# Optimization experiments

Measured on AMD Instinct MI355X. Metric: run time of the kernel, lower is better.

Reference implementation:

```python
import jax, jax.numpy as jnp
import numpy as np

# ---- fixed sizes ----
N_IN = 100_000          # total inner nodes
NODES_PER_INNER = 50    # nodes per inner graph
N_OUT = N_IN // NODES_PER_INNER          # 2000 outer nodes (= num inner graphs)
NODES_PER_OUTER = 125   # outer nodes per outer graph
B = N_OUT // NODES_PER_OUTER             # 16 graphs in the batch
DEG = 8
E_IN = N_IN * DEG        # 800_000 inner edges
E_OUT = N_OUT * DEG      # 16_000 outer edges
IN_FEATS = 64
OUT_FEATS = 64
H = 128                  # h_feats = [128]*6
NUM_CLASSES = 10


def _rand_edges(key, n_graphs, nodes_per_graph, edges_per_graph):
    """Random edges that stay inside each graph of a batched graph."""
    k1, k2 = jax.random.split(key)
    src_l = jax.random.randint(k1, (n_graphs, edges_per_graph), 0, nodes_per_graph)
    dst_l = jax.random.randint(k2, (n_graphs, edges_per_graph), 0, nodes_per_graph)
    off = (jnp.arange(n_graphs) * nodes_per_graph)[:, None]
    return ((src_l + off).reshape(-1).astype(jnp.int32),
            (dst_l + off).reshape(-1).astype(jnp.int32))


def setup_inputs() -> dict:
    key = jax.random.key(0)
    ks = jax.random.split(key, 24)
    inner_src, inner_dst = _rand_edges(ks[0], N_OUT, NODES_PER_INNER, E_IN // N_OUT)
    outer_src, outer_dst = _rand_edges(ks[1], B, NODES_PER_OUTER, E_OUT // B)

    def w(k, fan_in, fan_out):
        return jax.random.normal(k, (fan_in, fan_out), jnp.float32) * (1.0 / np.sqrt(fan_in))

    inp = {
        "in_layer_feat": jax.random.normal(ks[2], (N_IN, IN_FEATS), jnp.float32),
        "out_layer_feat": jax.random.normal(ks[3], (N_OUT, OUT_FEATS), jnp.float32),
        "inner_ew": jax.random.uniform(ks[4], (E_IN,), jnp.float32) + 0.5,
        "outer_ew": jax.random.uniform(ks[5], (E_OUT,), jnp.float32) + 0.5,
        "W1": w(ks[6], IN_FEATS, H),        "b1": jnp.zeros((H,), jnp.float32),
        "W2": w(ks[7], H, H),               "b2": jnp.zeros((H,), jnp.float32),
        "W3": w(ks[8], OUT_FEATS + H, H),   "b3": jnp.zeros((H,), jnp.float32),
        "W4": w(ks[9], H, H),               "b4": jnp.zeros((H,), jnp.float32),
        "W5": w(ks[10], H, H),              "b5": jnp.zeros((H,), jnp.float32),
        "W6": w(ks[11], H, H),              "b6": jnp.zeros((H,), jnp.float32),
        "Wc": w(ks[12], H, NUM_CLASSES),    "bc": jnp.zeros((NUM_CLASSES,), jnp.float32),
        "inner_src": inner_src, "inner_dst": inner_dst,
        "outer_src": outer_src, "outer_dst": outer_dst,
        "inner_node_graph": (jnp.arange(N_IN) // NODES_PER_INNER).astype(jnp.int32),
        "outer_node_graph": (jnp.arange(N_OUT) // NODES_PER_OUTER).astype(jnp.int32),
    }
    return inp


def graph_conv(src, dst, ew, x, W, b, n_nodes):
    """DGL GraphConv, norm='both', weighted aggregation, zero-in-degree allowed."""
    ones = jnp.ones(src.shape[0], x.dtype)
    deg_out = jnp.clip(jax.ops.segment_sum(ones, src, num_segments=n_nodes), 1.0)
    deg_in = jnp.clip(jax.ops.segment_sum(ones, dst, num_segments=n_nodes), 1.0)
    xs = x * jax.lax.rsqrt(deg_out)[:, None]                      # src normalization
    msg = xs[src] * ew[:, None]                                   # u_mul_e
    agg = jax.ops.segment_sum(msg, dst, num_segments=n_nodes)     # copy_e -> sum
    agg = agg * jax.lax.rsqrt(deg_in)[:, None]                    # dst normalization
    return agg @ W + b


def mean_nodes(h, node_graph, n_graphs, nodes_per_graph):
    return jax.ops.segment_sum(h, node_graph, num_segments=n_graphs) / nodes_per_graph


def reference(in_layer_feat, out_layer_feat, inner_ew, outer_ew,
              W1, b1, W2, b2, W3, b3, W4, b4, W5, b5, W6, b6, Wc, bc,
              inner_src, inner_dst, outer_src, outer_dst,
              inner_node_graph, outer_node_graph):
    # inner-graph message passing
    h = jax.nn.relu(graph_conv(inner_src, inner_dst, inner_ew, in_layer_feat, W1, b1, N_IN))
    h = jax.nn.relu(graph_conv(inner_src, inner_dst, inner_ew, h, W2, b2, N_IN))
    reduced = mean_nodes(h, inner_node_graph, N_OUT, float(NODES_PER_INNER))  # [N_OUT, H]
    merged = jnp.concatenate([out_layer_feat, reduced], axis=-1)              # [N_OUT, OUT_FEATS+H]
    # outer-graph message passing
    h = jax.nn.relu(graph_conv(outer_src, outer_dst, outer_ew, merged, W3, b3, N_OUT))
    h = jax.nn.relu(graph_conv(outer_src, outer_dst, outer_ew, h, W4, b4, N_OUT))
    h = jax.nn.relu(graph_conv(outer_src, outer_dst, outer_ew, h, W5, b5, N_OUT))
    h = jax.nn.relu(graph_conv(outer_src, outer_dst, outer_ew, h, W6, b6, N_OUT))
    hg = mean_nodes(h, outer_node_graph, B, float(NODES_PER_OUTER))           # [B, H]
    return hg @ Wc + bc                                                       # [B, NUM_CLASSES]
```

## Files before the change

### kernel.cpp

```cpp
#include <hip/hip_runtime.h>

#define NPI 50
#define EPI 400
#define NPO 125
#define EPO 1000
#define N_IN 100000
#define N_OUT 2000
#define NB 16
#define NC 10

typedef _Float16 half_t;
typedef _Float16 f16x8 __attribute__((ext_vector_type(8)));
typedef float f32x4 __attribute__((ext_vector_type(4)));

#define MFMA(a, b, c) __builtin_amdgcn_mfma_f32_16x16x32_f16(a, b, c, 0, 0, 0)

__device__ __forceinline__ void lds_barrier() {
    asm volatile("s_waitcnt lgkmcnt(0)" ::: "memory");
    __builtin_amdgcn_s_barrier();
}

__device__ __forceinline__ f16x8 lds_ld8(const half_t* base, int row, int k, int strideB) {
    return *(const f16x8*)((const char*)base + row * strideB + ((k * 2) ^ ((row & 7) << 4)));
}
__device__ __forceinline__ void lds_st1(half_t* base, int row, int col, int strideB, float v) {
    *(half_t*)((char*)base + row * strideB + ((col * 2) ^ ((row & 7) << 4))) = (half_t)v;
}
__device__ __forceinline__ void lds_st1h(half_t* base, int row, int col, int strideB, half_t v) {
    *(half_t*)((char*)base + row * strideB + ((col * 2) ^ ((row & 7) << 4))) = v;
}
__device__ __forceinline__ f16x8 scrS_ld8(const half_t* base, int row, int k, int strideB) {
    return *(const f16x8*)((const char*)base + row * strideB + ((k * 2) ^ ((row & 3) << 4)));
}
__device__ __forceinline__ void scrS_st1(half_t* base, int row, int col, int strideB, float v) {
    *(half_t*)((char*)base + row * strideB + ((col * 2) ^ ((row & 3) << 4))) = (half_t)v;
}

__global__ __launch_bounds__(256) void k_pre(
    const float* __restrict__ W1, const float* __restrict__ W2,
    const float* __restrict__ W3, const float* __restrict__ W4,
    const float* __restrict__ W5, const float* __restrict__ W6,
    half_t* __restrict__ WT1, half_t* __restrict__ WT2,
    half_t* __restrict__ WT3, half_t* __restrict__ WT4,
    half_t* __restrict__ WT5, half_t* __restrict__ WT6,
    const float* __restrict__ ew, const int* __restrict__ esrc,
    const int* __restrict__ edst, half_t* __restrict__ Aout)
{
    __shared__ float Af[NPO * NPO];
    __shared__ int cO[NPO], cI[NPO];
    __shared__ float rso[NPO], rsi[NPO];
    const int t = threadIdx.x;

    if (blockIdx.x < 384) {
        int i = blockIdx.x * 256 + t;
        const float* src; half_t* dst; int K;
        if      (i < 8192)  { src = W1; dst = WT1; K = 64; }
        else if (i < 24576) { src = W2; dst = WT2; K = 128; i -= 8192; }
        else if (i < 49152) { src = W3; dst = WT3; K = 192; i -= 24576; }
        else if (i < 65536) { src = W4; dst = WT4; K = 128; i -= 49152; }
        else if (i < 81920) { src = W5; dst = WT5; K = 128; i -= 65536; }
        else                { src = W6; dst = WT6; K = 128; i -= 81920; }
        int c = i & 127, k = i >> 7;
        dst[c * K + k] = (half_t)src[k * 128 + c];
        return;
    }

    const int g = blockIdx.x - 384;
    const int nb = g * NPO, eb = g * EPO;
    for (int i = t; i < NPO * NPO; i += 256) Af[i] = 0.f;
    if (t < NPO) { cO[t] = 0; cI[t] = 0; }
    __syncthreads();
    for (int e = t; e < EPO; e += 256) {
        int s = esrc[eb + e] - nb, d = edst[eb + e] - nb;
        atomicAdd(&Af[d * NPO + s], ew[eb + e]);
        atomicAdd(&cO[s], 1); atomicAdd(&cI[d], 1);
    }
    __syncthreads();
    if (t < NPO) {
        rso[t] = rsqrtf((float)max(cO[t], 1));
        rsi[t] = rsqrtf((float)max(cI[t], 1));
    }
    __syncthreads();
    for (int i = t; i < 128 * 16; i += 256) {
        int d = i >> 4, s0 = (i & 15) * 8;
        f16x8 v;
        #pragma unroll
        for (int j = 0; j < 8; j++) {
            int s = s0 + j;
            float x = (d < NPO && s < NPO) ? Af[d * NPO + s] * rsi[d] * rso[s] : 0.f;
            v[j] = (half_t)x;
        }
        *(f16x8*)&Aout[(size_t)g * 16384 + d * 128 + s0] = v;
    }
}

__global__ __launch_bounds__(256, 5) void k_inner(
    const float* __restrict__ X, const float* __restrict__ outfeat,
    const float* __restrict__ ew, const int* __restrict__ esrc,
    const int* __restrict__ edst,
    const half_t* __restrict__ WT1, const float* __restrict__ b1,
    const half_t* __restrict__ WT2, const float* __restrict__ b2,
    half_t* __restrict__ mergedT)
{
    __shared__ alignas(16) char smem[21504];
    half_t* R2  = (half_t*)smem;
    float*  Af  = (float*)smem;
    half_t* scr = (half_t*)(smem + 16384);
    float*  pool= (float*)(smem + 20480);
    int*    cO  = (int*)(smem + 20992);
    int*    cI  = (int*)(smem + 21248);

    const int g = blockIdx.x, t = threadIdx.x;
    const int w = t >> 6, l = t & 63, lr = l & 15, lk = l >> 4;
    const int nb = g * NPI, eb = g * EPI;
    half_t* scrw = scr + w * 512;

    float ofv = (t < 64) ? outfeat[(size_t)g * 64 + t] : 0.f;
    int s0e, d0e; float w0e;
    { int e = eb + t; s0e = esrc[e] - nb; d0e = edst[e] - nb; w0e = ew[e]; }
    int s1e = 0, d1e = 0; float w1e = 0.f;
    const bool e1v = (t + 256 < EPI);
    if (e1v) { int e = eb + t + 256; s1e = esrc[e] - nb; d1e = edst[e] - nb; w1e = ew[e]; }
    const int srow = t >> 2, qc = t & 3;
    f16x8 xh0 = {}, xh1 = {};
    if (srow < NPI) {
        const float* xp = &X[(size_t)(nb + srow) * 64 + qc * 16];
        float4 a = *(const float4*)(xp + 0), b = *(const float4*)(xp + 4);
        float4 c = *(const float4*)(xp + 8), d = *(const float4*)(xp + 12);
        xh0[0]=(half_t)a.x; xh0[1]=(half_t)a.y; xh0[2]=(half_t)a.z; xh0[3]=(half_t)a.w;
        xh0[4]=(half_t)b.x; xh0[5]=(half_t)b.y; xh0[6]=(half_t)b.z; xh0[7]=(half_t)b.w;
        xh1[0]=(half_t)c.x; xh1[1]=(half_t)c.y; xh1[2]=(half_t)c.z; xh1[3]=(half_t)c.w;
        xh1[4]=(half_t)d.x; xh1[5]=(half_t)d.y; xh1[6]=(half_t)d.z; xh1[7]=(half_t)d.w;
    }

    if (t < 64) { cO[t] = 0; cI[t] = 0; }
    if (t >= 64 && t < 192) pool[t - 64] = 0.f;
    for (int i = t; i < 4096; i += 256) Af[i] = 0.f;
    lds_barrier();

    atomicAdd(&Af[d0e * 64 + (s0e ^ ((d0e & 7) << 2))], w0e);
    atomicAdd(&cO[s0e], 1); atomicAdd(&cI[d0e], 1);
    if (e1v) {
        atomicAdd(&Af[d1e * 64 + (s1e ^ ((d1e & 7) << 2))], w1e);
        atomicAdd(&cO[s1e], 1); atomicAdd(&cI[d1e], 1);
    }
    lds_barrier();

    f16x8 afr[2];
    {
        const int r = w * 16 + lr;
        const int sw = (r & 7) << 2;
        const float rsi_l = rsqrtf((float)max(cI[r], 1));
        #pragma unroll
        for (int ks = 0; ks < 2; ks++) {
            const int c0 = ks * 32 + lk * 8;
            f32x4 v0 = *(const f32x4*)&Af[r * 64 + (c0 ^ sw)];
            f32x4 v1 = *(const f32x4*)&Af[r * 64 + ((c0 + 4) ^ sw)];
            f16x8 fr;
            #pragma unroll
            for (int j = 0; j < 4; j++)
                fr[j] = (half_t)(v0[j] * rsi_l * rsqrtf((float)max(cO[c0 + j], 1)));
            #pragma unroll
            for (int j = 0; j < 4; j++)
                fr[4 + j] = (half_t)(v1[j] * rsi_l * rsqrtf((float)max(cO[c0 + 4 + j], 1)));
            afr[ks] = fr;
        }
    }
    lds_barrier();

    #pragma unroll
    for (int i = 0; i < 8; i++) lds_st1h(R2, qc * 16 + i, srow, 128, xh0[i]);
    #pragma unroll
    for (int i = 0; i < 8; i++) lds_st1h(R2, qc * 16 + 8 + i, srow, 128, xh1[i]);
    lds_barrier();

    f32x4 hacc[8] = {};
    #pragma unroll
    for (int kf = 0; kf < 2; kf++) {
        f16x8 wb[8];
        #pragma unroll
        for (int nt = 0; nt < 8; nt++)
            wb[nt] = *(const f16x8*)&WT1[(nt * 16 + lr) * 64 + kf * 32 + lk * 8];
        #pragma unroll
        for (int j = 0; j < 2; j++) {
            const int ft = kf * 2 + j;
            f32x4 tacc = {};
            #pragma unroll
            for (int ks = 0; ks < 2; ks++) {
                f16x8 b = lds_ld8(R2, ft * 16 + lr, ks * 32 + lk * 8, 128);
                tacc = MFMA(afr[ks], b, tacc);
            }
            #pragma unroll
            for (int q = 0; q < 4; q++) scrS_st1(scrw, lk * 4 + q, j * 16 + lr, 64, tacc[q]);
        }
        f16x8 a1 = scrS_ld8(scrw, lr, lk * 8, 64);
        #pragma unroll
        for (int nt = 0; nt < 8; nt++) hacc[nt] = MFMA(a1, wb[nt], hacc[nt]);
    }
    lds_barrier();
    #pragma unroll
    for (int nt = 0; nt < 8; nt++) {
        int c = nt * 16 + lr;
        float bb = b1[c];
        #pragma unroll
        for (int q = 0; q < 4; q++)
            lds_st1(R2, c, w * 16 + lk * 4 + q, 128, fmaxf(hacc[nt][q] + bb, 0.f));
    }
    lds_barrier();

    f32x4 h2[8] = {};
    #pragma unroll
    for (int kf = 0; kf < 4; kf++) {
        f16x8 wb[8];
        #pragma unroll
        for (int nt = 0; nt < 8; nt++)
            wb[nt] = *(const f16x8*)&WT2[(nt * 16 + lr) * 128 + kf * 32 + lk * 8];
        #pragma unroll
        for (int j = 0; j < 2; j++) {
            const int ft = kf * 2 + j;
            f32x4 tacc = {};
            #pragma unroll
            for (int ks = 0; ks < 2; ks++) {
                f16x8 b = lds_ld8(R2, ft * 16 + lr, ks * 32 + lk * 8, 128);
                tacc = MFMA(afr[ks], b, tacc);
            }
            #pragma unroll
            for (int q = 0; q < 4; q++) scrS_st1(scrw, lk * 4 + q, j * 16 + lr, 64, tacc[q]);
        }
        f16x8 a1 = scrS_ld8(scrw, lr, lk * 8, 64);
        #pragma unroll
        for (int nt = 0; nt < 8; nt++) h2[nt] = MFMA(a1, wb[nt], h2[nt]);
    }
    #pragma unroll
    for (int nt = 0; nt < 8; nt++) {
        int c = nt * 16 + lr;
        float bb = b2[c];
        float ps = 0.f;
        #pragma unroll
        for (int q = 0; q < 4; q++) {
            int m = w * 16 + lk * 4 + q;
            float v = fmaxf(h2[nt][q] + bb, 0.f);
            ps += (m < NPI) ? v : 0.f;
        }
        ps += __shfl_xor(ps, 16);
        ps += __shfl_xor(ps, 32);
        if (lk == 0) atomicAdd(&pool[c], ps);
    }
    lds_barrier();
    {
        const int og = g / NPO, n = g - og * NPO;
        half_t* mT = mergedT + (size_t)og * 192 * 128 + n;
        if (t < 64) mT[(size_t)t * 128] = (half_t)ofv;
        else if (t < 192) mT[(size_t)t * 128] = (half_t)(pool[t - 64] * (1.f / NPI));
    }
}

template <int FIN>
__global__ __launch_bounds__(64) void k_layer(
    const half_t* __restrict__ Aout, const half_t* __restrict__ inT,
    const half_t* __restrict__ WT, const float* __restrict__ bias,
    half_t* __restrict__ outT)
{
    __shared__ alignas(16) half_t scrT[16 * FIN];
    __shared__ alignas(16) half_t hts[128 * 16];
    const int t = threadIdx.x, lr = t & 15, lk = t >> 4;
    const int og = blockIdx.x >> 3, r0 = (blockIdx.x & 7) * 16;
    const half_t* Ag = Aout + (size_t)og * 16384;
    const half_t* ig = inT + (size_t)og * FIN * 128;

    f16x8 af[4];
    #pragma unroll
    for (int ks = 0; ks < 4; ks++)
        af[ks] = *(const f16x8*)&Ag[(size_t)(r0 + lr) * 128 + ks * 32 + lk * 8];

    constexpr int NT = FIN / 16;
    #pragma unroll
    for (int nt = 0; nt < NT; nt++) {
        f32x4 tacc = {};
        #pragma unroll
        for (int ks = 0; ks < 4; ks++) {
            f16x8 b = *(const f16x8*)&ig[(size_t)(nt * 16 + lr) * 128 + ks * 32 + lk * 8];
            tacc = MFMA(af[ks], b, tacc);
        }
        #pragma unroll
        for (int q = 0; q < 4; q++)
            scrS_st1(scrT, lk * 4 + q, nt * 16 + lr, FIN * 2, tacc[q]);
    }

    f32x4 hacc[8] = {};
    #pragma unroll
    for (int ks2 = 0; ks2 < FIN / 32; ks2++) {
        f16x8 a1 = scrS_ld8(scrT, lr, ks2 * 32 + lk * 8, FIN * 2);
        #pragma unroll
        for (int nt2 = 0; nt2 < 8; nt2++) {
            f16x8 wb = *(const f16x8*)&WT[(size_t)(nt2 * 16 + lr) * FIN + ks2 * 32 + lk * 8];
            hacc[nt2] = MFMA(a1, wb, hacc[nt2]);
        }
    }
    #pragma unroll
    for (int nt2 = 0; nt2 < 8; nt2++) {
        int c = nt2 * 16 + lr;
        float bb = bias[c];
        #pragma unroll
        for (int q = 0; q < 4; q++)
            hts[c * 16 + lk * 4 + q] = (half_t)fmaxf(hacc[nt2][q] + bb, 0.f);
    }
    #pragma unroll
    for (int j = 0; j < 4; j++) {
        int id = t + j * 64;
        int f = id >> 1, i0 = (id & 1) * 8;
        f16x8 v = *(const f16x8*)&hts[f * 16 + i0];
        *(f16x8*)&outT[(size_t)og * 16384 + (size_t)f * 128 + r0 + i0] = v;
    }
}

__global__ __launch_bounds__(128) void k_pool(
    const half_t* __restrict__ h6T, const float* __restrict__ Wc,
    const float* __restrict__ bc, float* __restrict__ out)
{
    __shared__ float cls[NC];
    const int og = blockIdx.x, t = threadIdx.x;
    if (t < NC) cls[t] = 0.f;
    const half_t* hp = h6T + (size_t)og * 16384 + (size_t)t * 128;
    float s = 0.f;
    #pragma unroll
    for (int i = 0; i < 15; i++) {
        f16x8 v = *(const f16x8*)&hp[i * 8];
        #pragma unroll
        for (int j = 0; j < 8; j++) s += (float)v[j];
    }
    #pragma unroll
    for (int i = 120; i < 125; i++) s += (float)hp[i];
    const float val = s * (1.f / NPO);
    __syncthreads();
    {
        float p[NC];
        #pragma unroll
        for (int c = 0; c < NC; c++) p[c] = val * Wc[t * NC + c];
        #pragma unroll
        for (int off = 32; off >= 1; off >>= 1)
            #pragma unroll
            for (int c = 0; c < NC; c++) p[c] += __shfl_xor(p[c], off);
        if ((t & 63) == 0)
            #pragma unroll
            for (int c = 0; c < NC; c++) atomicAdd(&cls[c], p[c]);
    }
    __syncthreads();
    if (t < NC) out[og * NC + t] = cls[t] + bc[t];
}

extern "C" void kernel_launch(void* const* d_in, const int* in_sizes, int n_in,
                              void* d_out, int out_size, void* d_ws, size_t ws_size,
                              hipStream_t stream)
{
    const float* X       = (const float*)d_in[0];
    const float* outfeat = (const float*)d_in[1];
    const float* iew     = (const float*)d_in[2];
    const float* oew     = (const float*)d_in[3];
    const float* W1 = (const float*)d_in[4];  const float* b1 = (const float*)d_in[5];
    const float* W2 = (const float*)d_in[6];  const float* b2 = (const float*)d_in[7];
    const float* W3 = (const float*)d_in[8];  const float* b3 = (const float*)d_in[9];
    const float* W4 = (const float*)d_in[10]; const float* b4 = (const float*)d_in[11];
    const float* W5 = (const float*)d_in[12]; const float* b5 = (const float*)d_in[13];
    const float* W6 = (const float*)d_in[14]; const float* b6 = (const float*)d_in[15];
    const float* Wc = (const float*)d_in[16]; const float* bc = (const float*)d_in[17];
    const int* isrc = (const int*)d_in[18];   const int* idst = (const int*)d_in[19];
    const int* osrc = (const int*)d_in[20];   const int* odst = (const int*)d_in[21];

    char* base = (char*)d_ws;
    half_t* WT1 = (half_t*)(base + 0);
    half_t* WT2 = (half_t*)(base + 16384);
    half_t* WT3 = (half_t*)(base + 49152);
    half_t* WT4 = (half_t*)(base + 98304);
    half_t* WT5 = (half_t*)(base + 131072);
    half_t* WT6 = (half_t*)(base + 163840);
    half_t* AoutG   = (half_t*)(base + 196608);
    half_t* mergedT = (half_t*)(base + 720896);
    half_t* hTa     = (half_t*)(base + 1507328);
    half_t* hTb     = (half_t*)(base + 2031616);

    k_pre<<<400, 256, 0, stream>>>(W1, W2, W3, W4, W5, W6,
                                   WT1, WT2, WT3, WT4, WT5, WT6,
                                   oew, osrc, odst, AoutG);
    k_inner<<<N_OUT, 256, 0, stream>>>(X, outfeat, iew, isrc, idst,
                                       WT1, b1, WT2, b2, mergedT);
    k_layer<192><<<NB * 8, 64, 0, stream>>>(AoutG, mergedT, WT3, b3, hTa);
    k_layer<128><<<NB * 8, 64, 0, stream>>>(AoutG, hTa, WT4, b4, hTb);
    k_layer<128><<<NB * 8, 64, 0, stream>>>(AoutG, hTb, WT5, b5, hTa);
    k_layer<128><<<NB * 8, 64, 0, stream>>>(AoutG, hTa, WT6, b6, hTb);
    k_pool<<<NB, 128, 0, stream>>>(hTb, Wc, bc, (float*)d_out);
}
```

Before: 135.3 us.

## Fuse outer-graph layers and pooling into one persistent kernel with grid barriers

Replaces the four per-layer launches and the pooling launch with a single persistent 128-block kernel that uses global atomic-counter barriers between stages. The outer adjacency build and the W3-W6 transposes move into this kernel, and the adjacency is accumulated in global memory that a small pre-kernel zeroes. Each block now uses 4 waves, each computing a quarter of the output columns instead of one wave doing all of them. The aim is to remove several kernel launch gaps and tails on a short dependent chain, at the cost of spin-barrier overhead and global atomics for the adjacency.

```diff
diff --git a/kernel.cpp b/kernel.cpp
--- a/kernel.cpp
+++ b/kernel.cpp
@@ -8,6 +8,7 @@
 #define N_OUT 2000
 #define NB 16
 #define NC 10
+#define OB 128
 
 typedef _Float16 half_t;
 typedef _Float16 f16x8 __attribute__((ext_vector_type(8)));
@@ -36,62 +37,21 @@
     *(half_t*)((char*)base + row * strideB + ((col * 2) ^ ((row & 3) << 4))) = (half_t)v;
 }
 
-__global__ __launch_bounds__(256) void k_pre(
+__global__ __launch_bounds__(256) void k_preW12(
     const float* __restrict__ W1, const float* __restrict__ W2,
-    const float* __restrict__ W3, const float* __restrict__ W4,
-    const float* __restrict__ W5, const float* __restrict__ W6,
     half_t* __restrict__ WT1, half_t* __restrict__ WT2,
-    half_t* __restrict__ WT3, half_t* __restrict__ WT4,
-    half_t* __restrict__ WT5, half_t* __restrict__ WT6,
-    const float* __restrict__ ew, const int* __restrict__ esrc,
-    const int* __restrict__ edst, half_t* __restrict__ Aout)
+    int* __restrict__ zbase, int zcount)
 {
-    __shared__ float Af[NPO * NPO];
-    __shared__ int cO[NPO], cI[NPO];
-    __shared__ float rso[NPO], rsi[NPO];
-    const int t = threadIdx.x;
-
-    if (blockIdx.x < 384) {
-        int i = blockIdx.x * 256 + t;
-        const float* src; half_t* dst; int K;
-        if      (i < 8192)  { src = W1; dst = WT1; K = 64; }
-        else if (i < 24576) { src = W2; dst = WT2; K = 128; i -= 8192; }
-        else if (i < 49152) { src = W3; dst = WT3; K = 192; i -= 24576; }
-        else if (i < 65536) { src = W4; dst = WT4; K = 128; i -= 49152; }
-        else if (i < 81920) { src = W5; dst = WT5; K = 128; i -= 65536; }
-        else                { src = W6; dst = WT6; K = 128; i -= 81920; }
+    int i = blockIdx.x * 256 + threadIdx.x;
+    if (i < 8192) {
         int c = i & 127, k = i >> 7;
-        dst[c * K + k] = (half_t)src[k * 128 + c];
-        return;
-    }
-
-    const int g = blockIdx.x - 384;
-    const int nb = g * NPO, eb = g * EPO;
-    for (int i = t; i < NPO * NPO; i += 256) Af[i] = 0.f;
-    if (t < NPO) { cO[t] = 0; cI[t] = 0; }
-    __syncthreads();
-    for (int e = t; e < EPO; e += 256) {
-        int s = esrc[eb + e] - nb, d = edst[eb + e] - nb;
-        atomicAdd(&Af[d * NPO + s], ew[eb + e]);
-        atomicAdd(&cO[s], 1); atomicAdd(&cI[d], 1);
-    }
-    __syncthreads();
-    if (t < NPO) {
-        rso[t] = rsqrtf((float)max(cO[t], 1));
-        rsi[t] = rsqrtf((float)max(cI[t], 1));
-    }
-    __syncthreads();
-    for (int i = t; i < 128 * 16; i += 256) {
-        int d = i >> 4, s0 = (i & 15) * 8;
-        f16x8 v;
-        #pragma unroll
-        for (int j = 0; j < 8; j++) {
-            int s = s0 + j;
-            float x = (d < NPO && s < NPO) ? Af[d * NPO + s] * rsi[d] * rso[s] : 0.f;
-            v[j] = (half_t)x;
-        }
-        *(f16x8*)&Aout[(size_t)g * 16384 + d * 128 + s0] = v;
-    }
+        WT1[c * 64 + k] = (half_t)W1[k * 128 + c];
+    } else {
+        int ii = i - 8192;
+        int c = ii & 127, k = ii >> 7;
+        WT2[c * 128 + k] = (half_t)W2[k * 128 + c];
+    }
+    for (int j = i; j < zcount; j += 96 * 256) zbase[j] = 0;
 }
 
 __global__ __launch_bounds__(256, 5) void k_inner(
@@ -255,98 +215,177 @@
     }
 }
 
+__device__ __forceinline__ void gsync(int* ctr, int idx) {
+    __syncthreads();
+    if (threadIdx.x == 0) {
+        __threadfence();
+        atomicAdd(&ctr[idx], 1);
+        while (atomicAdd(&ctr[idx], 0) < OB) __builtin_amdgcn_s_sleep(2);
+        __threadfence();
+    }
+    __syncthreads();
+}
+
 template <int FIN>
-__global__ __launch_bounds__(64) void k_layer(
-    const half_t* __restrict__ Aout, const half_t* __restrict__ inT,
+__device__ __forceinline__ void do_layer(
+    const f16x8* af, const half_t* __restrict__ ig,
     const half_t* __restrict__ WT, const float* __restrict__ bias,
-    half_t* __restrict__ outT)
+    half_t* __restrict__ outg, int r0, half_t* scrT, half_t* hts,
+    int w, int lr, int lk, int t)
 {
-    __shared__ alignas(16) half_t scrT[16 * FIN];
-    __shared__ alignas(16) half_t hts[128 * 16];
-    const int t = threadIdx.x, lr = t & 15, lk = t >> 4;
-    const int og = blockIdx.x >> 3, r0 = (blockIdx.x & 7) * 16;
-    const half_t* Ag = Aout + (size_t)og * 16384;
-    const half_t* ig = inT + (size_t)og * FIN * 128;
-
-    f16x8 af[4];
-    #pragma unroll
-    for (int ks = 0; ks < 4; ks++)
-        af[ks] = *(const f16x8*)&Ag[(size_t)(r0 + lr) * 128 + ks * 32 + lk * 8];
-
-    constexpr int NT = FIN / 16;
-    #pragma unroll
-    for (int nt = 0; nt < NT; nt++) {
+    constexpr int TP = FIN / 64;
+    #pragma unroll
+    for (int tt = 0; tt < TP; tt++) {
+        const int ft = w * TP + tt;
         f32x4 tacc = {};
         #pragma unroll
         for (int ks = 0; ks < 4; ks++) {
-            f16x8 b = *(const f16x8*)&ig[(size_t)(nt * 16 + lr) * 128 + ks * 32 + lk * 8];
+            f16x8 b = *(const f16x8*)&ig[(size_t)(ft * 16 + lr) * 128 + ks * 32 + lk * 8];
             tacc = MFMA(af[ks], b, tacc);
         }
         #pragma unroll
         for (int q = 0; q < 4; q++)
-            scrS_st1(scrT, lk * 4 + q, nt * 16 + lr, FIN * 2, tacc[q]);
-    }
-
-    f32x4 hacc[8] = {};
+            scrS_st1(scrT, lk * 4 + q, ft * 16 + lr, FIN * 2, tacc[q]);
+    }
+    __syncthreads();
+    f32x4 hacc[2] = {};
     #pragma unroll
     for (int ks2 = 0; ks2 < FIN / 32; ks2++) {
         f16x8 a1 = scrS_ld8(scrT, lr, ks2 * 32 + lk * 8, FIN * 2);
         #pragma unroll
-        for (int nt2 = 0; nt2 < 8; nt2++) {
-            f16x8 wb = *(const f16x8*)&WT[(size_t)(nt2 * 16 + lr) * FIN + ks2 * 32 + lk * 8];
+        for (int nt2 = 0; nt2 < 2; nt2++) {
+            f16x8 wb = *(const f16x8*)&WT[(size_t)(w * 32 + nt2 * 16 + lr) * FIN
+                                          + ks2 * 32 + lk * 8];
             hacc[nt2] = MFMA(a1, wb, hacc[nt2]);
         }
     }
     #pragma unroll
-    for (int nt2 = 0; nt2 < 8; nt2++) {
-        int c = nt2 * 16 + lr;
+    for (int nt2 = 0; nt2 < 2; nt2++) {
+        int c = w * 32 + nt2 * 16 + lr;
         float bb = bias[c];
         #pragma unroll
         for (int q = 0; q < 4; q++)
             hts[c * 16 + lk * 4 + q] = (half_t)fmaxf(hacc[nt2][q] + bb, 0.f);
     }
-    #pragma unroll
-    for (int j = 0; j < 4; j++) {
-        int id = t + j * 64;
-        int f = id >> 1, i0 = (id & 1) * 8;
-        f16x8 v = *(const f16x8*)&hts[f * 16 + i0];
-        *(f16x8*)&outT[(size_t)og * 16384 + (size_t)f * 128 + r0 + i0] = v;
-    }
-}
-
-__global__ __launch_bounds__(128) void k_pool(
-    const half_t* __restrict__ h6T, const float* __restrict__ Wc,
-    const float* __restrict__ bc, float* __restrict__ out)
-{
-    __shared__ float cls[NC];
-    const int og = blockIdx.x, t = threadIdx.x;
-    if (t < NC) cls[t] = 0.f;
-    const half_t* hp = h6T + (size_t)og * 16384 + (size_t)t * 128;
-    float s = 0.f;
-    #pragma unroll
-    for (int i = 0; i < 15; i++) {
-        f16x8 v = *(const f16x8*)&hp[i * 8];
-        #pragma unroll
-        for (int j = 0; j < 8; j++) s += (float)v[j];
-    }
-    #pragma unroll
-    for (int i = 120; i < 125; i++) s += (float)hp[i];
-    const float val = s * (1.f / NPO);
     __syncthreads();
     {
-        float p[NC];
-        #pragma unroll
-        for (int c = 0; c < NC; c++) p[c] = val * Wc[t * NC + c];
-        #pragma unroll
-        for (int off = 32; off >= 1; off >>= 1)
-            #pragma unroll
-            for (int c = 0; c < NC; c++) p[c] += __shfl_xor(p[c], off);
-        if ((t & 63) == 0)
-            #pragma unroll
-            for (int c = 0; c < NC; c++) atomicAdd(&cls[c], p[c]);
+        int f = t >> 1, i0 = (t & 1) * 8;
+        f16x8 v = *(const f16x8*)&hts[f * 16 + i0];
+        *(f16x8*)&outg[(size_t)f * 128 + r0 + i0] = v;
     }
     __syncthreads();
-    if (t < NC) out[og * NC + t] = cls[t] + bc[t];
+}
+
+__global__ __launch_bounds__(256) void k_outer_one(
+    const float* __restrict__ W3, const float* __restrict__ W4,
+    const float* __restrict__ W5, const float* __restrict__ W6,
+    half_t* __restrict__ WT3, half_t* __restrict__ WT4,
+    half_t* __restrict__ WT5, half_t* __restrict__ WT6,
+    const float* __restrict__ ewo, const int* __restrict__ esrc,
+    const int* __restrict__ edst,
+    float* __restrict__ AfG, int* __restrict__ cOG, int* __restrict__ cIG,
+    half_t* __restrict__ Aout, const half_t* __restrict__ mergedT,
+    const float* __restrict__ b3, const float* __restrict__ b4,
+    const float* __restrict__ b5, const float* __restrict__ b6,
+    half_t* __restrict__ hT1, half_t* __restrict__ hT2,
+    half_t* __restrict__ hT3, half_t* __restrict__ hT4,
+    const float* __restrict__ Wc, const float* __restrict__ bc,
+    int* __restrict__ ctr, float* __restrict__ out)
+{
+    __shared__ alignas(16) half_t scrT[16 * 192];
+    __shared__ alignas(16) half_t hts[128 * 16];
+    __shared__ float cls[NC];
+    const int bid = blockIdx.x, t = threadIdx.x;
+    const int w = t >> 6, l = t & 63, lr = l & 15, lk = l >> 4;
+
+    for (int i = bid * 256 + t; i < 73728; i += OB * 256) {
+        const float* src; half_t* dst; int K, ii;
+        if (i < 24576) { src = W3; dst = WT3; K = 192; ii = i; }
+        else {
+            int r = i - 24576, m = r >> 14;
+            ii = r & 16383; K = 128;
+            src = (m == 0) ? W4 : (m == 1) ? W5 : W6;
+            dst = (m == 0) ? WT4 : (m == 1) ? WT5 : WT6;
+        }
+        int c = ii & 127, k = ii >> 7;
+        dst[c * K + k] = (half_t)src[k * 128 + c];
+    }
+    if (bid < NB) {
+        const int g = bid, nb = g * NPO, eb = g * EPO;
+        float* Afg = AfG + (size_t)g * (NPO * NPO);
+        int* cO = cOG + g * NPO; int* cI = cIG + g * NPO;
+        for (int e = t; e < EPO; e += 256) {
+            int s = esrc[eb + e] - nb, d = edst[eb + e] - nb;
+            atomicAdd(&Afg[d * NPO + s], ewo[eb + e]);
+            atomicAdd(&cO[s], 1); atomicAdd(&cI[d], 1);
+        }
+        __threadfence();
+        __syncthreads();
+        for (int i = t; i < 128 * 16; i += 256) {
+            int d = i >> 4, s0 = (i & 15) * 8;
+            float rsi_l = (d < NPO) ? rsqrtf((float)max(cI[d], 1)) : 0.f;
+            f16x8 v;
+            #pragma unroll
+            for (int j = 0; j < 8; j++) {
+                int s = s0 + j;
+                float x = (d < NPO && s < NPO)
+                    ? Afg[d * NPO + s] * rsi_l * rsqrtf((float)max(cO[s], 1)) : 0.f;
+                v[j] = (half_t)x;
+            }
+            *(f16x8*)&Aout[(size_t)g * 16384 + d * 128 + s0] = v;
+        }
+    }
+    gsync(ctr, 0);
+
+    const int og = bid >> 3, r0 = (bid & 7) * 16;
+    f16x8 af[4];
+    #pragma unroll
+    for (int ks = 0; ks < 4; ks++)
+        af[ks] = *(const f16x8*)&Aout[(size_t)og * 16384 + (size_t)(r0 + lr) * 128
+                                      + ks * 32 + lk * 8];
+
+    do_layer<192>(af, mergedT + (size_t)og * 192 * 128, WT3, b3,
+                  hT1 + (size_t)og * 16384, r0, scrT, hts, w, lr, lk, t);
+    gsync(ctr, 1);
+    do_layer<128>(af, hT1 + (size_t)og * 16384, WT4, b4,
+                  hT2 + (size_t)og * 16384, r0, scrT, hts, w, lr, lk, t);
+    gsync(ctr, 2);
+    do_layer<128>(af, hT2 + (size_t)og * 16384, WT5, b5,
+                  hT3 + (size_t)og * 16384, r0, scrT, hts, w, lr, lk, t);
+    gsync(ctr, 3);
+    do_layer<128>(af, hT3 + (size_t)og * 16384, WT6, b6,
+                  hT4 + (size_t)og * 16384, r0, scrT, hts, w, lr, lk, t);
+    gsync(ctr, 4);
+
+    if (bid < NB) {
+        if (t < NC) cls[t] = 0.f;
+        __syncthreads();
+        if (t < 128) {
+            const half_t* hp = hT4 + (size_t)bid * 16384 + (size_t)t * 128;
+            float s = 0.f;
+            #pragma unroll
+            for (int i = 0; i < 15; i++) {
+                f16x8 v = *(const f16x8*)&hp[i * 8];
+                #pragma unroll
+                for (int j = 0; j < 8; j++) s += (float)v[j];
+            }
+            #pragma unroll
+            for (int i = 120; i < 125; i++) s += (float)hp[i];
+            const float val = s * (1.f / NPO);
+            float p[NC];
+            #pragma unroll
+            for (int c = 0; c < NC; c++) p[c] = val * Wc[t * NC + c];
+            #pragma unroll
+            for (int off = 32; off >= 1; off >>= 1)
+                #pragma unroll
+                for (int c = 0; c < NC; c++) p[c] += __shfl_xor(p[c], off);
+            if ((t & 63) == 0)
+                #pragma unroll
+                for (int c = 0; c < NC; c++) atomicAdd(&cls[c], p[c]);
+        }
+        __syncthreads();
+        if (t < NC) out[bid * NC + t] = cls[t] + bc[t];
+    }
 }
 
 extern "C" void kernel_launch(void* const* d_in, const int* in_sizes, int n_in,
@@ -376,17 +415,23 @@
     half_t* WT6 = (half_t*)(base + 163840);
     half_t* AoutG   = (half_t*)(base + 196608);
     half_t* mergedT = (half_t*)(base + 720896);
-    half_t* hTa     = (half_t*)(base + 1507328);
-    half_t* hTb     = (half_t*)(base + 2031616);
-
-    k_pre<<<400, 256, 0, stream>>>(W1, W2, W3, W4, W5, W6,
-                                   WT1, WT2, WT3, WT4, WT5, WT6,
-                                   oew, osrc, odst, AoutG);
+    half_t* hT1 = (half_t*)(base + 1507328);
+    half_t* hT2 = (half_t*)(base + 2031616);
+    half_t* hT3 = (half_t*)(base + 2555904);
+    half_t* hT4 = (half_t*)(base + 3080192);
+    int*    ctr = (int*)(base + 3604480);
+    float*  AfG = (float*)(base + 3604608);
+    int*    cOG = (int*)(base + 4604608);
+    int*    cIG = (int*)(base + 4612608);
+    int*    zbase = (int*)(base + 3604480);
+    const int zcount = (4620608 - 3604480) / 4;
+
+    k_preW12<<<96, 256, 0, stream>>>(W1, W2, WT1, WT2, zbase, zcount);
     k_inner<<<N_OUT, 256, 0, stream>>>(X, outfeat, iew, isrc, idst,
                                        WT1, b1, WT2, b2, mergedT);
-    k_layer<192><<<NB * 8, 64, 0, stream>>>(AoutG, mergedT, WT3, b3, hTa);
-    k_layer<128><<<NB * 8, 64, 0, stream>>>(AoutG, hTa, WT4, b4, hTb);
-    k_layer<128><<<NB * 8, 64, 0, stream>>>(AoutG, hTb, WT5, b5, hTa);
-    k_layer<128><<<NB * 8, 64, 0, stream>>>(AoutG, hTa, WT6, b6, hTb);
-    k_pool<<<NB, 128, 0, stream>>>(hTb, Wc, bc, (float*)d_out);
-}
+    k_outer_one<<<OB, 256, 0, stream>>>(W3, W4, W5, W6, WT3, WT4, WT5, WT6,
+                                        oew, osrc, odst, AfG, cOG, cIG,
+                                        AoutG, mergedT, b3, b4, b5, b6,
+                                        hT1, hT2, hT3, hT4, Wc, bc, ctr,
+                                        (float*)d_out);
+}
```

After: 167.4 us. +23.7%, slower.
